# Performance work log

Hardware: AMD Instinct MI355X
Metric: run time of the kernel (lower is better)

The kernel has to match this reference:

```python
import jax, jax.numpy as jnp
import numpy as np


def _gtconv(A, w):
    # A: [E,N,N], w: [C,E,1,1]; torch: sum(A * softmax(w, dim=1), dim=1) -> [C,N,N]
    s = jax.nn.softmax(w[:, :, 0, 0], axis=1)  # [C,E]
    return jnp.einsum('enm,ce->cnm', A, s)


def _norm_row(H):
    # row-normalize (H + I): D^-1 (H + I)
    n = H.shape[0]
    H = H + jnp.eye(n, dtype=H.dtype)
    deg = jnp.sum(H, axis=1)
    deg = jnp.where(deg <= 1e-10, 1.0, deg)
    return H / deg[:, None]


def _sgc(feature, adj):
    # D^-1/2 (adj + 2I) D^-1/2 @ feature  (diag scaling, same math as torch's dense mm with diag)
    n = adj.shape[0]
    adj = adj + 2.0 * jnp.eye(n, dtype=adj.dtype)
    deg = jnp.sum(adj, axis=1)
    deg = jnp.where(deg <= 1e-10, 1.0, deg)
    dinv = deg ** -0.5
    adj = adj * dinv[:, None] * dinv[None, :]
    return adj @ feature


def setup_inputs() -> dict:
    key = jax.random.key(0)
    ks = jax.random.split(key, 20)
    E, C, N, D, P, F = 5, 2, 3000, 1000, 2000, 128
    inp = {
        'A': jax.random.uniform(ks[0], (E, N, N), dtype=jnp.float32),
        'DTI': jax.random.uniform(ks[1], (N, N), dtype=jnp.float32),
        'drug_structure': jax.random.normal(ks[2], (D, F), dtype=jnp.float32),
        'protein_structure': jax.random.normal(ks[3], (P, F), dtype=jnp.float32),
        'gt_w0a': jax.random.normal(ks[4], (C, E, 1, 1), dtype=jnp.float32),
        'gt_w0b': jax.random.normal(ks[5], (C, E, 1, 1), dtype=jnp.float32),
        'gt_w1': jax.random.normal(ks[6], (C, E, 1, 1), dtype=jnp.float32),
        'a_param': jnp.ones((C + 1, 1, 1), dtype=jnp.float32),
        'drug_num': D,
        'protein_num': P,
    }
    lin_keys = jax.random.split(ks[7], 12)
    names = ['wd1', 'bd1', 'wd2', 'bd2', 'wd3', 'bd3', 'wp1', 'bp1', 'wp2', 'bp2', 'wp3', 'bp3']
    for i, nm in enumerate(names):
        shp = (F, F) if nm.startswith('w') else (F,)
        inp[nm] = jax.random.normal(lin_keys[i], shp, dtype=jnp.float32) * 0.05
    return inp


def reference(A, DTI, drug_structure, protein_structure, gt_w0a, gt_w0b, gt_w1,
              wd1, bd1, wd2, bd2, wd3, bd3, wp1, bp1, wp2, bp2, wp3, bp3,
              a_param, drug_num, protein_num):
    relu = jax.nn.relu
    drug = relu(drug_structure @ wd1.T + bd1)
    drug = relu(drug @ wd2.T + bd2)
    drug = relu(drug @ wd3.T + bd3)
    prot = relu(protein_structure @ wp1.T + bp1)
    prot = relu(prot @ wp2.T + bp2)
    prot = relu(prot @ wp3.T + bp3)
    feature = jnp.concatenate([drug, prot], axis=0)  # [N,128]

    # GT layers: layer 0 (first=True), layer 1 (first=False)
    a0 = _gtconv(A, gt_w0a)  # [C,N,N]
    b0 = _gtconv(A, gt_w0b)
    H = jnp.matmul(a0, b0)  # bmm
    H = jax.vmap(_norm_row)(H)
    H = jnp.matmul(H, _gtconv(A, gt_w1))

    adj = H  # H[:, :N, :N] is a no-op here
    X_conv1 = _sgc(_sgc(feature, DTI), DTI)
    chs = jax.vmap(lambda a_: _sgc(_sgc(feature, a_), a_))(adj)  # [C,N,128]

    C = adj.shape[0]
    if C == 1:
        X_conv3 = chs
    else:
        order = [0, 1]
        for i in range(2, C):
            order = [i] + order  # torch prepends X_tem for i>=2
        X_conv3 = chs[jnp.array(order)]

    X_conv = jnp.concatenate([X_conv1[None], X_conv3], axis=0)  # [C+1,N,128]
    att = jax.nn.softmax(a_param, axis=0)  # [C+1,1,1]
    conv_sum = jnp.sum(att * X_conv, axis=0)  # [N,128]

    drug_feature = conv_sum[:drug_num]
    protein_feature = conv_sum[drug_num:]
    y = jax.nn.sigmoid(drug_feature @ protein_feature.T)  # [D,P]
    return y
```

## Files before the change

### kernel.cpp

```cpp
#include <hip/hip_runtime.h>
#include <hip/hip_bf16.h>

typedef __attribute__((ext_vector_type(8))) __bf16 bf16x8;
typedef __attribute__((ext_vector_type(4))) float floatx4;

#define NVALID 3000
#define NPAD   3072
#define FEA    128
#define ZSPLIT 8
#define KCHUNK 384
#define PSTRIDE 393216
#define SLOT   ((size_t)ZSPLIT * PSTRIDE)

__device__ __forceinline__ void gload16(const void* g, void* l) {
    __builtin_amdgcn_global_load_lds(
        (const __attribute__((address_space(1))) void*)g,
        (__attribute__((address_space(3))) void*)l,
        16, 0, 0);
}

__device__ __forceinline__ float b2f(__hip_bfloat16 h) { return __bfloat162float(h); }

__global__ __launch_bounds__(256) void mlp_fused(
    const float* __restrict__ Xd, const float* __restrict__ Xp,
    const float* __restrict__ Wd1, const float* __restrict__ bd1,
    const float* __restrict__ Wd2, const float* __restrict__ bd2,
    const float* __restrict__ Wd3, const float* __restrict__ bd3,
    const float* __restrict__ Wp1, const float* __restrict__ bp1,
    const float* __restrict__ Wp2, const float* __restrict__ bp2,
    const float* __restrict__ Wp3, const float* __restrict__ bp3,
    float* __restrict__ Y)
{
    const bool isP = blockIdx.x >= 125;
    const float* X  = isP ? Xp : Xd;
    const float* W1 = isP ? Wp1 : Wd1; const float* b1 = isP ? bp1 : bd1;
    const float* W2 = isP ? Wp2 : Wd2; const float* b2 = isP ? bp2 : bd2;
    const float* W3 = isP ? Wp3 : Wd3; const float* b3 = isP ? bp3 : bd3;
    const int m0loc = (isP ? (blockIdx.x - 125) : blockIdx.x) * 8;
    const int m0out = blockIdx.x * 8;

    __shared__ float S0[8][128], S1[8][128];
    const int t = threadIdx.x;
    for (int s2 = t; s2 < 1024; s2 += 256) {
        int r = s2 >> 7, ii = s2 & 127;
        S0[r][ii] = X[(size_t)(m0loc + r) * 128 + ii];
    }
    __syncthreads();
    const int o = t & 127, rh = t >> 7;

    {
        float a0 = 0.f, a1 = 0.f, a2 = 0.f, a3 = 0.f;
        const float* wr = W1 + (size_t)o * 128;
        for (int i = 0; i < 128; ++i) {
            float w = wr[i];
            a0 += S0[rh + 0][i] * w; a1 += S0[rh + 2][i] * w;
            a2 += S0[rh + 4][i] * w; a3 += S0[rh + 6][i] * w;
        }
        float bo = b1[o];
        S1[rh + 0][o] = fmaxf(a0 + bo, 0.f);
        S1[rh + 2][o] = fmaxf(a1 + bo, 0.f);
        S1[rh + 4][o] = fmaxf(a2 + bo, 0.f);
        S1[rh + 6][o] = fmaxf(a3 + bo, 0.f);
    }
    __syncthreads();
    {
        float a0 = 0.f, a1 = 0.f, a2 = 0.f, a3 = 0.f;
        const float* wr = W2 + (size_t)o * 128;
        for (int i = 0; i < 128; ++i) {
            float w = wr[i];
            a0 += S1[rh + 0][i] * w; a1 += S1[rh + 2][i] * w;
            a2 += S1[rh + 4][i] * w; a3 += S1[rh + 6][i] * w;
        }
        float bo = b2[o];
        S0[rh + 0][o] = fmaxf(a0 + bo, 0.f);
        S0[rh + 2][o] = fmaxf(a1 + bo, 0.f);
        S0[rh + 4][o] = fmaxf(a2 + bo, 0.f);
        S0[rh + 6][o] = fmaxf(a3 + bo, 0.f);
    }
    __syncthreads();
    {
        float a0 = 0.f, a1 = 0.f, a2 = 0.f, a3 = 0.f;
        const float* wr = W3 + (size_t)o * 128;
        for (int i = 0; i < 128; ++i) {
            float w = wr[i];
            a0 += S0[rh + 0][i] * w; a1 += S0[rh + 2][i] * w;
            a2 += S0[rh + 4][i] * w; a3 += S0[rh + 6][i] * w;
        }
        float bo = b3[o];
        Y[(size_t)(m0out + rh + 0) * 128 + o] = fmaxf(a0 + bo, 0.f);
        Y[(size_t)(m0out + rh + 2) * 128 + o] = fmaxf(a1 + bo, 0.f);
        Y[(size_t)(m0out + rh + 4) * 128 + o] = fmaxf(a2 + bo, 0.f);
        Y[(size_t)(m0out + rh + 6) * 128 + o] = fmaxf(a3 + bo, 0.f);
    }
}

__device__ __forceinline__ void softmax5(const float* __restrict__ w, float* s)
{
    float m = w[0];
    #pragma unroll
    for (int e = 1; e < 5; ++e) m = fmaxf(m, w[e]);
    float sum = 0.f;
    #pragma unroll
    for (int e = 0; e < 5; ++e) { s[e] = __expf(w[e] - m); sum += s[e]; }
    float r = 1.f / sum;
    #pragma unroll
    for (int e = 0; e < 5; ++e) s[e] *= r;
}

__global__ __launch_bounds__(384) void gtconv_fused(
    const float* __restrict__ A, const float* __restrict__ w0a,
    const float* __restrict__ w0b, const float* __restrict__ w1,
    __hip_bfloat16* __restrict__ a00, __hip_bfloat16* __restrict__ b00,
    __hip_bfloat16* __restrict__ g10,
    __hip_bfloat16* __restrict__ a01, __hip_bfloat16* __restrict__ b01,
    __hip_bfloat16* __restrict__ g11,
    float* __restrict__ r1v)
{
    float sw[6][5];
    softmax5(w0a + 0, sw[0]); softmax5(w0b + 0, sw[1]); softmax5(w1 + 0, sw[2]);
    softmax5(w0a + 5, sw[3]); softmax5(w0b + 5, sw[4]); softmax5(w1 + 5, sw[5]);

    const int i  = blockIdx.x;
    const int t  = threadIdx.x;
    const int j0 = t * 8;
    float acc[6][8] = {};
    if (i < NVALID && j0 < NVALID) {
        #pragma unroll
        for (int e = 0; e < 5; ++e) {
            const float* Ae = A + (size_t)e * 9000000 + (size_t)i * 3000 + j0;
            float4 v0 = *reinterpret_cast<const float4*>(Ae);
            float4 v1 = *reinterpret_cast<const float4*>(Ae + 4);
            float x[8] = { v0.x, v0.y, v0.z, v0.w, v1.x, v1.y, v1.z, v1.w };
            #pragma unroll
            for (int m = 0; m < 6; ++m) {
                float se = sw[m][e];
                #pragma unroll
                for (int u = 0; u < 8; ++u) acc[m][u] += se * x[u];
            }
        }
    }
    __hip_bfloat16* dsts[6] = { a00, b00, g10, a01, b01, g11 };
    const size_t base = (size_t)i * NPAD + j0;
    float rs[4];
    #pragma unroll
    for (int m = 0; m < 6; ++m) {
        __align__(16) __hip_bfloat16 h[8];
        float s = 0.f;
        #pragma unroll
        for (int u = 0; u < 8; ++u) {
            h[u] = __float2bfloat16(acc[m][u]);
            s += b2f(h[u]);
        }
        *reinterpret_cast<uint4*>(&dsts[m][base]) = *reinterpret_cast<const uint4*>(h);
        if (m == 1) rs[0] = s; else if (m == 2) rs[1] = s;
        else if (m == 4) rs[2] = s; else if (m == 5) rs[3] = s;
    }
    __shared__ float red[6][4];
    #pragma unroll
    for (int q = 0; q < 4; ++q) {
        float s = rs[q];
        #pragma unroll
        for (int off = 32; off > 0; off >>= 1) s += __shfl_down(s, off);
        if ((t & 63) == 0) red[t >> 6][q] = s;
    }
    __syncthreads();
    if (t == 0) {
        #pragma unroll
        for (int q = 0; q < 4; ++q) {
            float s = red[0][q] + red[1][q] + red[2][q]
                    + red[3][q] + red[4][q] + red[5][q];
            r1v[(size_t)q * NPAD + i] = s;
        }
    }
}

__global__ __launch_bounds__(256) void matvec_degA(
    const __hip_bfloat16* __restrict__ a0_0, const __hip_bfloat16* __restrict__ a0_1,
    const __hip_bfloat16* __restrict__ b0_0, const __hip_bfloat16* __restrict__ b0_1,
    const float* __restrict__ r1v,
    float* __restrict__ dinv2, float* __restrict__ mv12)
{
    const int y = blockIdx.y;
    const __hip_bfloat16* M = (y == 0) ? a0_0 : (y == 1) ? a0_1 : (y == 2) ? b0_0 : b0_1;
    const float* v = (y == 0) ? r1v : (y == 1) ? r1v + 2 * NPAD
                   : (y == 2) ? r1v + NPAD : r1v + 3 * NPAD;
    const size_t i = blockIdx.x;
    const int t = threadIdx.x;
    const __hip_bfloat16* row = M + i * NPAD;
    float s = 0.f;
    for (int k = t * 8; k < NPAD; k += 2048) {
        uint4 u = *reinterpret_cast<const uint4*>(&row[k]);
        const unsigned short* us = reinterpret_cast<const unsigned short*>(&u);
        #pragma unroll
        for (int e = 0; e < 8; ++e)
            s += __uint_as_float(((unsigned int)us[e]) << 16) * v[k + e];
    }
    #pragma unroll
    for (int off = 32; off > 0; off >>= 1) s += __shfl_down(s, off);
    __shared__ float red[4];
    if ((t & 63) == 0) red[t >> 6] = s;
    __syncthreads();
    if (t == 0) {
        float tot = red[0] + red[1] + red[2] + red[3];
        if (y < 2) dinv2[(size_t)y * NPAD + i] = 1.f / (tot + 1.f);
        else       mv12[(size_t)(y - 2) * NPAD + i] = tot;
    }
}

__global__ __launch_bounds__(256) void matvec_degB(
    const __hip_bfloat16* __restrict__ a0_0, const __hip_bfloat16* __restrict__ a0_1,
    const float* __restrict__ mv12, const float* __restrict__ dinv2,
    const float* __restrict__ r1v, float* __restrict__ rsv2)
{
    const int c = blockIdx.y;
    const __hip_bfloat16* M = c ? a0_1 : a0_0;
    const float* v = mv12 + (size_t)c * NPAD;
    const float* add = r1v + (size_t)(2 * c + 1) * NPAD;
    const size_t i = blockIdx.x;
    const int t = threadIdx.x;
    const __hip_bfloat16* row = M + i * NPAD;
    float s = 0.f;
    for (int k = t * 8; k < NPAD; k += 2048) {
        uint4 u = *reinterpret_cast<const uint4*>(&row[k]);
        const unsigned short* us = reinterpret_cast<const unsigned short*>(&u);
        #pragma unroll
        for (int e = 0; e < 8; ++e)
            s += __uint_as_float(((unsigned int)us[e]) << 16) * v[k + e];
    }
    #pragma unroll
    for (int off = 32; off > 0; off >>= 1) s += __shfl_down(s, off);
    __shared__ float red[4];
    if ((t & 63) == 0) red[t >> 6] = s;
    __syncthreads();
    if (t == 0) {
        float tot = red[0] + red[1] + red[2] + red[3];
        rsv2[(size_t)c * NPAD + i] =
            rsqrtf(dinv2[(size_t)c * NPAD + i] * (tot + add[i]) + 2.f);
    }
}

__global__ __launch_bounds__(256) void rowdeg_f32(
    const float* __restrict__ src, float* __restrict__ outv)
{
    const int i = blockIdx.x, t = threadIdx.x;
    float s = 0.f;
    if (i < NVALID) {
        const float* row = src + (size_t)i * 3000;
        for (int j4 = t; j4 < 750; j4 += 256) {
            float4 v = *reinterpret_cast<const float4*>(row + j4 * 4);
            s += v.x + v.y + v.z + v.w;
        }
    }
    #pragma unroll
    for (int off = 32; off > 0; off >>= 1) s += __shfl_down(s, off);
    __shared__ float red[4];
    if ((t & 63) == 0) red[t >> 6] = s;
    __syncthreads();
    if (t == 0) {
        float tot = red[0] + red[1] + red[2] + red[3];
        outv[i] = rsqrtf(tot + 2.f);
    }
}

__global__ __launch_bounds__(256) void scale_cast_f32(
    const float* __restrict__ src, int lds_, int nvalid,
    const float* __restrict__ vec, __hip_bfloat16* __restrict__ dst)
{
    const int i = blockIdx.y;
    const int j0 = (blockIdx.x * 256 + threadIdx.x) * 4;
    const float vi = vec[i];
    float v[4];
    if (i < nvalid && j0 + 3 < nvalid) {
        float4 f = *reinterpret_cast<const float4*>(src + (size_t)i * lds_ + j0);
        v[0] = f.x; v[1] = f.y; v[2] = f.z; v[3] = f.w;
    } else {
        #pragma unroll
        for (int u = 0; u < 4; ++u) {
            int j = j0 + u;
            v[u] = (i < nvalid && j < nvalid) ? src[(size_t)i * lds_ + j] : 0.f;
        }
    }
    #pragma unroll
    for (int u = 0; u < 4; ++u) {
        int j = j0 + u;
        if (j == i && i < nvalid) v[u] += 2.f;
        v[u] *= vi * vec[j];
    }
    __align__(8) __hip_bfloat16 h[4];
    #pragma unroll
    for (int u = 0; u < 4; ++u) h[u] = __float2bfloat16(v[u]);
    *reinterpret_cast<uint2*>(&dst[(size_t)i * NPAD + j0]) =
        *reinterpret_cast<const uint2*>(h);
}

__global__ __launch_bounds__(256) void transpose_feat(
    const float* __restrict__ X, int nvalid, __hip_bfloat16* __restrict__ XT)
{
    __shared__ float Ts[32][33];
    const int k0 = blockIdx.x * 32, n0 = blockIdx.y * 32;
    const int t = threadIdx.x, tr = t >> 5, tc = t & 31;
    #pragma unroll
    for (int p = 0; p < 4; ++p) {
        int k = k0 + tr + p * 8;
        Ts[tr + p * 8][tc] = (k < nvalid) ? X[(size_t)k * 128 + n0 + tc] : 0.f;
    }
    __syncthreads();
    #pragma unroll
    for (int p = 0; p < 4; ++p) {
        int n = tr + p * 8;
        XT[(size_t)(n0 + n) * NPAD + k0 + tc] = __float2bfloat16(Ts[tc][n]);
    }
}

__global__ __launch_bounds__(256) void scale_colsT2(
    const __hip_bfloat16* __restrict__ XT, const float* __restrict__ rsv2,
    __hip_bfloat16* __restrict__ W0T_0, __hip_bfloat16* __restrict__ W0T_1)
{
    const int c = blockIdx.z;
    const float* s = rsv2 + (size_t)c * NPAD;
    __hip_bfloat16* W0T = c ? W0T_1 : W0T_0;
    const int f = blockIdx.y;
    const int k0 = (blockIdx.x * 256 + threadIdx.x) * 8;
    if (k0 >= NPAD) return;
    uint4 u = *reinterpret_cast<const uint4*>(&XT[(size_t)f * NPAD + k0]);
    const unsigned short* us = reinterpret_cast<const unsigned short*>(&u);
    __align__(16) __hip_bfloat16 h[8];
    #pragma unroll
    for (int e = 0; e < 8; ++e) {
        float x = __uint_as_float(((unsigned int)us[e]) << 16);
        h[e] = __float2bfloat16(x * s[k0 + e]);
    }
    *reinterpret_cast<uint4*>(&W0T[(size_t)f * NPAD + k0]) =
        *reinterpret_cast<const uint4*>(h);
}

__global__ __launch_bounds__(256, 3) void gemm_bt_batch(
    const __hip_bfloat16* __restrict__ A0, const __hip_bfloat16* __restrict__ B0,
    const __hip_bfloat16* __restrict__ A1, const __hip_bfloat16* __restrict__ B1,
    const __hip_bfloat16* __restrict__ A2, const __hip_bfloat16* __restrict__ B2,
    __hip_bfloat16* __restrict__ part)
{
    const int b  = blockIdx.z / ZSPLIT;
    const int zz = blockIdx.z % ZSPLIT;
    const __hip_bfloat16* A  = (b == 0) ? A0 : (b == 1) ? A1 : A2;
    const __hip_bfloat16* BT = (b == 0) ? B0 : (b == 1) ? B1 : B2;
    __hip_bfloat16* C = part + (size_t)b * SLOT + (size_t)zz * PSTRIDE;

    __shared__ __align__(16) __hip_bfloat16 As[128 * 32];
    __shared__ __align__(16) __hip_bfloat16 Bs[128 * 32];
    const int t = threadIdx.x;
    const int lane = t & 63;
    const int w = t >> 6;
    const int wm = w >> 1, wn = w & 1;
    const int tm = blockIdx.y;
    const int kbeg = zz * KCHUNK;

    const int srow = lane >> 2;
    const int skg  = (lane & 3) * 8;
    const __hip_bfloat16* Ag = A  + (size_t)(tm * 128 + w * 32 + srow) * NPAD + skg;
    const __hip_bfloat16* Bg = BT + (size_t)(w * 32 + srow) * NPAD + skg;
    __hip_bfloat16* Al0 = &As[w * 1024];
    __hip_bfloat16* Al1 = &As[w * 1024 + 512];
    __hip_bfloat16* Bl0 = &Bs[w * 1024];
    __hip_bfloat16* Bl1 = &Bs[w * 1024 + 512];

    floatx4 acc[4][4] = {};

    for (int k0 = kbeg; k0 < kbeg + KCHUNK; k0 += 32) {
        __syncthreads();
        gload16(Ag + k0,             Al0);
        gload16(Ag + 16 * NPAD + k0, Al1);
        gload16(Bg + k0,             Bl0);
        gload16(Bg + 16 * NPAD + k0, Bl1);
        __syncthreads();

        bf16x8 af[4], bfv[4];
        const int koff = (lane >> 4) * 8;
        #pragma unroll
        for (int mi = 0; mi < 4; ++mi)
            af[mi] = *reinterpret_cast<const bf16x8*>(
                &As[(wm * 64 + mi * 16 + (lane & 15)) * 32 + koff]);
        #pragma unroll
        for (int ni = 0; ni < 4; ++ni)
            bfv[ni] = *reinterpret_cast<const bf16x8*>(
                &Bs[(wn * 64 + ni * 16 + (lane & 15)) * 32 + koff]);
        #pragma unroll
        for (int mi = 0; mi < 4; ++mi)
            #pragma unroll
            for (int ni = 0; ni < 4; ++ni)
                acc[mi][ni] = __builtin_amdgcn_mfma_f32_16x16x32_bf16(
                    af[mi], bfv[ni], acc[mi][ni], 0, 0, 0);
    }

    const int r0 = tm * 128 + wm * 64 + ((lane >> 4) << 2);
    const int c0 = wn * 64 + (lane & 15);
    #pragma unroll
    for (int mi = 0; mi < 4; ++mi)
        #pragma unroll
        for (int ni = 0; ni < 4; ++ni)
            #pragma unroll
            for (int r = 0; r < 4; ++r)
                C[(size_t)(r0 + mi * 16 + r) * 128 + c0 + ni * 16] =
                    __float2bfloat16(acc[mi][ni][r]);
}

__global__ __launch_bounds__(256, 3) void gemm_sig(
    const __hip_bfloat16* __restrict__ A, const __hip_bfloat16* __restrict__ BT,
    float* __restrict__ C, int Kchunk, int lda, int ldb, int ldc,
    int Mvalid, int Nvalid)
{
    __shared__ __align__(16) __hip_bfloat16 As[128 * 32];
    __shared__ __align__(16) __hip_bfloat16 Bs[128 * 32];
    const int t = threadIdx.x;
    const int lane = t & 63;
    const int w = t >> 6;
    const int wm = w >> 1, wn = w & 1;
    const int tm = blockIdx.y, tn = blockIdx.x;

    const int srow = lane >> 2;
    const int skg  = (lane & 3) * 8;
    const __hip_bfloat16* Ag = A  + (size_t)(tm * 128 + w * 32 + srow) * lda + skg;
    const __hip_bfloat16* Bg = BT + (size_t)(tn * 128 + w * 32 + srow) * ldb + skg;
    __hip_bfloat16* Al0 = &As[w * 1024];
    __hip_bfloat16* Al1 = &As[w * 1024 + 512];
    __hip_bfloat16* Bl0 = &Bs[w * 1024];
    __hip_bfloat16* Bl1 = &Bs[w * 1024 + 512];

    floatx4 acc[4][4] = {};

    for (int k0 = 0; k0 < Kchunk; k0 += 32) {
        __syncthreads();
        gload16(Ag + k0,            Al0);
        gload16(Ag + 16 * lda + k0, Al1);
        gload16(Bg + k0,            Bl0);
        gload16(Bg + 16 * ldb + k0, Bl1);
        __syncthreads();

        bf16x8 af[4], bfv[4];
        const int koff = (lane >> 4) * 8;
        #pragma unroll
        for (int mi = 0; mi < 4; ++mi)
            af[mi] = *reinterpret_cast<const bf16x8*>(
                &As[(wm * 64 + mi * 16 + (lane & 15)) * 32 + koff]);
        #pragma unroll
        for (int ni = 0; ni < 4; ++ni)
            bfv[ni] = *reinterpret_cast<const bf16x8*>(
                &Bs[(wn * 64 + ni * 16 + (lane & 15)) * 32 + koff]);
        #pragma unroll
        for (int mi = 0; mi < 4; ++mi)
            #pragma unroll
            for (int ni = 0; ni < 4; ++ni)
                acc[mi][ni] = __builtin_amdgcn_mfma_f32_16x16x32_bf16(
                    af[mi], bfv[ni], acc[mi][ni], 0, 0, 0);
    }

    const int r0 = tm * 128 + wm * 64 + ((lane >> 4) << 2);
    const int c0 = tn * 128 + wn * 64 + (lane & 15);
    #pragma unroll
    for (int mi = 0; mi < 4; ++mi)
        #pragma unroll
        for (int ni = 0; ni < 4; ++ni) {
            const int col = c0 + ni * 16;
            #pragma unroll
            for (int r = 0; r < 4; ++r) {
                const int row = r0 + mi * 16 + r;
                if (row < Mvalid && col < Nvalid)
                    C[(size_t)row * ldc + col] =
                        1.f / (1.f + __expf(-acc[mi][ni][r]));
            }
        }
}

__global__ __launch_bounds__(256) void reduce_trans_b(
    const __hip_bfloat16* __restrict__ part,
    __hip_bfloat16* __restrict__ X0, __hip_bfloat16* __restrict__ X1,
    __hip_bfloat16* __restrict__ X2,
    __hip_bfloat16* __restrict__ R0, __hip_bfloat16* __restrict__ R1,
    __hip_bfloat16* __restrict__ R2,
    const float* __restrict__ ap, float* __restrict__ conv)
{
    const int b = blockIdx.z;
    const __hip_bfloat16* Pp = part + (size_t)b * SLOT;
    const int k0 = blockIdx.x * 32, n0 = blockIdx.y * 32;
    const int t = threadIdx.x, tr = t >> 5, tc = t & 31;

    if (b == 0 && conv != nullptr) {
        float a0 = ap[0], a1 = ap[1], a2 = ap[2];
        float m = fmaxf(a0, fmaxf(a1, a2));
        float e0 = __expf(a0 - m), e1 = __expf(a1 - m), e2 = __expf(a2 - m);
        float att0 = e0 / (e0 + e1 + e2);
        #pragma unroll
        for (int p = 0; p < 4; ++p) {
            int i = k0 + tr + p * 8;
            float s = 0.f;
            #pragma unroll
            for (int z = 0; z < ZSPLIT; ++z)
                s += b2f(Pp[(size_t)z * PSTRIDE + (size_t)i * 128 + n0 + tc]);
            conv[(size_t)i * 128 + n0 + tc] = att0 * s;
        }
        return;
    }

    __hip_bfloat16* XT = (b == 0) ? X0 : (b == 1) ? X1 : X2;
    __hip_bfloat16* Rm = (b == 0) ? R0 : (b == 1) ? R1 : R2;
    __shared__ float Ts[32][33];
    #pragma unroll
    for (int p = 0; p < 4; ++p) {
        int i = k0 + tr + p * 8;
        float s = 0.f;
        #pragma unroll
        for (int z = 0; z < ZSPLIT; ++z)
            s += b2f(Pp[(size_t)z * PSTRIDE + (size_t)i * 128 + n0 + tc]);
        Ts[tr + p * 8][tc] = s;
        if (Rm) Rm[(size_t)i * 128 + n0 + tc] = __float2bfloat16(s);
    }
    __syncthreads();
    #pragma unroll
    for (int p = 0; p < 4; ++p) {
        int n = tr + p * 8;
        XT[(size_t)(n0 + n) * NPAD + k0 + tc] = __float2bfloat16(Ts[tc][n]);
    }
}

__global__ __launch_bounds__(256) void combine_mid2(
    const __hip_bfloat16* __restrict__ part,
    const __hip_bfloat16* __restrict__ Zrm0, const __hip_bfloat16* __restrict__ Zrm1,
    const float* __restrict__ X,
    const float* __restrict__ rsv2, const float* __restrict__ dinv2,
    __hip_bfloat16* __restrict__ WpT0, __hip_bfloat16* __restrict__ WpT1,
    __hip_bfloat16* __restrict__ Wprm0, __hip_bfloat16* __restrict__ Wprm1)
{
    const int c = blockIdx.z;
    const __hip_bfloat16* Vp = part + (size_t)c * SLOT;
    const __hip_bfloat16* Zrm = c ? Zrm1 : Zrm0;
    const float* sv = rsv2 + (size_t)c * NPAD;
    const float* dv = dinv2 + (size_t)c * NPAD;
    __hip_bfloat16* WpT  = c ? WpT1 : WpT0;
    __hip_bfloat16* Wprm = c ? Wprm1 : Wprm0;

    __shared__ float Ts[32][33];
    const int k0 = blockIdx.x * 32, n0 = blockIdx.y * 32;
    const int t = threadIdx.x, tr = t >> 5, tc = t & 31;
    #pragma unroll
    for (int p = 0; p < 4; ++p) {
        int i = k0 + tr + p * 8;
        int f = n0 + tc;
        float vsum = b2f(Zrm[(size_t)i * 128 + f]);
        #pragma unroll
        for (int z = 0; z < ZSPLIT; ++z)
            vsum += b2f(Vp[(size_t)z * PSTRIDE + (size_t)i * 128 + f]);
        float x  = (i < NVALID) ? X[(size_t)i * 128 + f] : 0.f;
        float si = sv[i];
        float out1 = si * dv[i] * vsum + 2.f * si * si * x;
        float wv = si * out1;
        Ts[tr + p * 8][tc] = wv;
        Wprm[(size_t)i * 128 + f] = __float2bfloat16(wv);
    }
    __syncthreads();
    #pragma unroll
    for (int p = 0; p < 4; ++p) {
        int n = tr + p * 8;
        WpT[(size_t)(n0 + n) * NPAD + k0 + tc] = __float2bfloat16(Ts[tc][n]);
    }
}

__global__ __launch_bounds__(256) void combine_att2(
    const __hip_bfloat16* __restrict__ part,
    const __hip_bfloat16* __restrict__ Zrm0, const __hip_bfloat16* __restrict__ Zrm1,
    const __hip_bfloat16* __restrict__ Wprm0, const __hip_bfloat16* __restrict__ Wprm1,
    const float* __restrict__ rsv2, const float* __restrict__ dinv2,
    const float* __restrict__ ap, float* __restrict__ conv)
{
    const int idx = blockIdx.x * 256 + threadIdx.x;
    const int i = idx >> 7;
    float v0 = b2f(Zrm0[idx]);
    float v1 = b2f(Zrm1[idx]);
    #pragma unroll
    for (int z = 0; z < ZSPLIT; ++z) {
        v0 += b2f(part[(size_t)z * PSTRIDE + idx]);
        v1 += b2f(part[SLOT + (size_t)z * PSTRIDE + idx]);
    }
    float s0 = rsv2[i],        d0 = dinv2[i];
    float s1 = rsv2[NPAD + i], d1 = dinv2[NPAD + i];
    float o0 = s0 * d0 * v0 + 2.f * s0 * b2f(Wprm0[idx]);
    float o1 = s1 * d1 * v1 + 2.f * s1 * b2f(Wprm1[idx]);
    float a0 = ap[0], a1 = ap[1], a2 = ap[2];
    float m = fmaxf(a0, fmaxf(a1, a2));
    float e0 = __expf(a0 - m), e1 = __expf(a1 - m), e2 = __expf(a2 - m);
    float inv = 1.f / (e0 + e1 + e2);
    conv[idx] += (e1 * inv) * o0 + (e2 * inv) * o1;
}

__global__ __launch_bounds__(256) void cast_split(
    const float* __restrict__ acc, __hip_bfloat16* __restrict__ dF,
    __hip_bfloat16* __restrict__ pF)
{
    const int idx = blockIdx.x * 256 + threadIdx.x;
    if (idx < 1024 * 128) {
        int r = idx >> 7;
        dF[idx] = __float2bfloat16(r < 1000 ? acc[idx] : 0.f);
    } else {
        int j = idx - 1024 * 128;
        int r = j >> 7;
        pF[j] = __float2bfloat16(r < 2000 ? acc[(size_t)(1000 + r) * 128 + (j & 127)] : 0.f);
    }
}

extern "C" void kernel_launch(void* const* d_in, const int* in_sizes, int n_in,
                              void* d_out, int out_size, void* d_ws, size_t ws_size,
                              hipStream_t stream)
{
    const float* A     = (const float*)d_in[0];
    const float* DTI   = (const float*)d_in[1];
    const float* drugS = (const float*)d_in[2];
    const float* protS = (const float*)d_in[3];
    const float* w0a   = (const float*)d_in[4];
    const float* w0b   = (const float*)d_in[5];
    const float* w1g   = (const float*)d_in[6];
    const float* ap    = (const float*)d_in[7];
    const float* wd1 = (const float*)d_in[10]; const float* bd1 = (const float*)d_in[11];
    const float* wd2 = (const float*)d_in[12]; const float* bd2 = (const float*)d_in[13];
    const float* wd3 = (const float*)d_in[14]; const float* bd3 = (const float*)d_in[15];
    const float* wp1 = (const float*)d_in[16]; const float* bp1 = (const float*)d_in[17];
    const float* wp2 = (const float*)d_in[18]; const float* bp2 = (const float*)d_in[19];
    const float* wp3 = (const float*)d_in[20]; const float* bp3 = (const float*)d_in[21];
    float* out = (float*)d_out;

    const size_t SQ_BF  = (size_t)NPAD * NPAD * 2;
    const size_t PAN_BF = (size_t)128 * NPAD * 2;
    char* p = (char*)d_ws;
    auto alloc = [&](size_t sz) { char* r = p; p += (sz + 255) & ~(size_t)255; return r; };
    __hip_bfloat16* sdti = (__hip_bfloat16*)alloc(SQ_BF);
    __hip_bfloat16* a0c[2], *b0c[2], *g1c[2];
    for (int c = 0; c < 2; ++c) {
        a0c[c] = (__hip_bfloat16*)alloc(SQ_BF);
        b0c[c] = (__hip_bfloat16*)alloc(SQ_BF);
        g1c[c] = (__hip_bfloat16*)alloc(SQ_BF);
    }
    __hip_bfloat16* part = (__hip_bfloat16*)alloc((size_t)3 * SLOT * 2);
    float* r1v   = (float*)alloc((size_t)4 * NPAD * 4);
    float* dinv2 = (float*)alloc((size_t)2 * NPAD * 4);
    float* mv12  = (float*)alloc((size_t)2 * NPAD * 4);
    float* rsv2  = (float*)alloc((size_t)2 * NPAD * 4);
    float* degv  = (float*)alloc((size_t)NPAD * 4);
    float* fb    = (float*)alloc((size_t)NPAD * 128 * 4);
    float* conv  = (float*)alloc((size_t)NPAD * 128 * 4);
    __hip_bfloat16* XTF  = (__hip_bfloat16*)alloc(PAN_BF);
    __hip_bfloat16* XT2  = (__hip_bfloat16*)alloc(PAN_BF);
    __hip_bfloat16* W0T_0 = (__hip_bfloat16*)alloc(PAN_BF);
    __hip_bfloat16* W0T_1 = (__hip_bfloat16*)alloc(PAN_BF);
    __hip_bfloat16* ZT_0  = (__hip_bfloat16*)alloc(PAN_BF);
    __hip_bfloat16* ZT_1  = (__hip_bfloat16*)alloc(PAN_BF);
    __hip_bfloat16* Zrm_0 = (__hip_bfloat16*)alloc(PAN_BF);
    __hip_bfloat16* Zrm_1 = (__hip_bfloat16*)alloc(PAN_BF);
    __hip_bfloat16* UT_0  = (__hip_bfloat16*)alloc(PAN_BF);
    __hip_bfloat16* UT_1  = (__hip_bfloat16*)alloc(PAN_BF);
    __hip_bfloat16* WpT_0 = (__hip_bfloat16*)alloc(PAN_BF);
    __hip_bfloat16* WpT_1 = (__hip_bfloat16*)alloc(PAN_BF);
    __hip_bfloat16* Wprm_0 = (__hip_bfloat16*)alloc(PAN_BF);
    __hip_bfloat16* Wprm_1 = (__hip_bfloat16*)alloc(PAN_BF);
    __hip_bfloat16* dF = (__hip_bfloat16*)alloc((size_t)1024 * 128 * 2);
    __hip_bfloat16* pF = (__hip_bfloat16*)alloc((size_t)2048 * 128 * 2);
    if ((size_t)(p - (char*)d_ws) > ws_size) return;

    mlp_fused<<<375, 256, 0, stream>>>(drugS, protS,
        wd1, bd1, wd2, bd2, wd3, bd3, wp1, bp1, wp2, bp2, wp3, bp3, fb);
    transpose_feat<<<dim3(96, 4), 256, 0, stream>>>(fb, 3000, XTF);

    gtconv_fused<<<NPAD, 384, 0, stream>>>(A, w0a, w0b, w1g,
        a0c[0], b0c[0], g1c[0], a0c[1], b0c[1], g1c[1], r1v);

    rowdeg_f32<<<NPAD, 256, 0, stream>>>(DTI, degv);
    scale_cast_f32<<<dim3(3, NPAD), 256, 0, stream>>>(DTI, 3000, 3000, degv, sdti);

    matvec_degA<<<dim3(NPAD, 4), 256, 0, stream>>>(a0c[0], a0c[1], b0c[0], b0c[1],
        r1v, dinv2, mv12);
    matvec_degB<<<dim3(NPAD, 2), 256, 0, stream>>>(a0c[0], a0c[1], mv12, dinv2, r1v, rsv2);
    scale_colsT2<<<dim3(2, 128, 2), 256, 0, stream>>>(XTF, rsv2, W0T_0, W0T_1);

    gemm_bt_batch<<<dim3(1, 24, 3 * ZSPLIT), 256, 0, stream>>>(
        sdti, XTF, g1c[0], W0T_0, g1c[1], W0T_1, part);
    reduce_trans_b<<<dim3(96, 4, 3), 256, 0, stream>>>(part,
        XT2, ZT_0, ZT_1, nullptr, Zrm_0, Zrm_1, nullptr, nullptr);

    gemm_bt_batch<<<dim3(1, 24, 3 * ZSPLIT), 256, 0, stream>>>(
        sdti, XT2, b0c[0], ZT_0, b0c[1], ZT_1, part);
    reduce_trans_b<<<dim3(96, 4, 3), 256, 0, stream>>>(part,
        nullptr, UT_0, UT_1, nullptr, nullptr, nullptr, ap, conv);

    gemm_bt_batch<<<dim3(1, 24, 2 * ZSPLIT), 256, 0, stream>>>(
        a0c[0], UT_0, a0c[1], UT_1, nullptr, nullptr, part);
    combine_mid2<<<dim3(96, 4, 2), 256, 0, stream>>>(part, Zrm_0, Zrm_1, fb,
        rsv2, dinv2, WpT_0, WpT_1, Wprm_0, Wprm_1);

    gemm_bt_batch<<<dim3(1, 24, 2 * ZSPLIT), 256, 0, stream>>>(
        g1c[0], WpT_0, g1c[1], WpT_1, nullptr, nullptr, part);
    reduce_trans_b<<<dim3(96, 4, 2), 256, 0, stream>>>(part,
        ZT_0, ZT_1, nullptr, Zrm_0, Zrm_1, nullptr, nullptr, nullptr);
    gemm_bt_batch<<<dim3(1, 24, 2 * ZSPLIT), 256, 0, stream>>>(
        b0c[0], ZT_0, b0c[1], ZT_1, nullptr, nullptr, part);
    reduce_trans_b<<<dim3(96, 4, 2), 256, 0, stream>>>(part,
        UT_0, UT_1, nullptr, nullptr, nullptr, nullptr, nullptr, nullptr);
    gemm_bt_batch<<<dim3(1, 24, 2 * ZSPLIT), 256, 0, stream>>>(
        a0c[0], UT_0, a0c[1], UT_1, nullptr, nullptr, part);
    combine_att2<<<1500, 256, 0, stream>>>(part, Zrm_0, Zrm_1, Wprm_0, Wprm_1,
        rsv2, dinv2, ap, conv);

    cast_split<<<1536, 256, 0, stream>>>(conv, dF, pF);
    gemm_sig<<<dim3(16, 8), 256, 0, stream>>>(dF, pF, out, 128, 128, 128, 2000, 1000, 2000);
}
```

Before: 269.8 us.

## Keep chain intermediates in transposed panel layout, drop per-step transposes

```diff
diff --git a/kernel.cpp b/kernel.cpp
--- a/kernel.cpp
+++ b/kernel.cpp
@@ -334,16 +334,16 @@
         *reinterpret_cast<const uint4*>(h);
 }
 
-__global__ __launch_bounds__(256, 3) void gemm_bt_batch(
-    const __hip_bfloat16* __restrict__ A0, const __hip_bfloat16* __restrict__ B0,
-    const __hip_bfloat16* __restrict__ A1, const __hip_bfloat16* __restrict__ B1,
-    const __hip_bfloat16* __restrict__ A2, const __hip_bfloat16* __restrict__ B2,
+__global__ __launch_bounds__(256, 3) void gemm_pan_batch(
+    const __hip_bfloat16* __restrict__ P0, const __hip_bfloat16* __restrict__ M0,
+    const __hip_bfloat16* __restrict__ P1, const __hip_bfloat16* __restrict__ M1,
+    const __hip_bfloat16* __restrict__ P2, const __hip_bfloat16* __restrict__ M2,
     __hip_bfloat16* __restrict__ part)
 {
     const int b  = blockIdx.z / ZSPLIT;
     const int zz = blockIdx.z % ZSPLIT;
-    const __hip_bfloat16* A  = (b == 0) ? A0 : (b == 1) ? A1 : A2;
-    const __hip_bfloat16* BT = (b == 0) ? B0 : (b == 1) ? B1 : B2;
+    const __hip_bfloat16* P = (b == 0) ? P0 : (b == 1) ? P1 : P2;
+    const __hip_bfloat16* M = (b == 0) ? M0 : (b == 1) ? M1 : M2;
     __hip_bfloat16* C = part + (size_t)b * SLOT + (size_t)zz * PSTRIDE;
 
     __shared__ __align__(16) __hip_bfloat16 As[128 * 32];
@@ -352,13 +352,13 @@
     const int lane = t & 63;
     const int w = t >> 6;
     const int wm = w >> 1, wn = w & 1;
-    const int tm = blockIdx.y;
+    const int tn = blockIdx.x;
     const int kbeg = zz * KCHUNK;
 
     const int srow = lane >> 2;
     const int skg  = (lane & 3) * 8;
-    const __hip_bfloat16* Ag = A  + (size_t)(tm * 128 + w * 32 + srow) * NPAD + skg;
-    const __hip_bfloat16* Bg = BT + (size_t)(w * 32 + srow) * NPAD + skg;
+    const __hip_bfloat16* Ag = P + (size_t)(w * 32 + srow) * NPAD + skg;
+    const __hip_bfloat16* Bg = M + (size_t)(tn * 128 + w * 32 + srow) * NPAD + skg;
     __hip_bfloat16* Al0 = &As[w * 1024];
     __hip_bfloat16* Al1 = &As[w * 1024 + 512];
     __hip_bfloat16* Bl0 = &Bs[w * 1024];
@@ -392,15 +392,15 @@
                     af[mi], bfv[ni], acc[mi][ni], 0, 0, 0);
     }
 
-    const int r0 = tm * 128 + wm * 64 + ((lane >> 4) << 2);
-    const int c0 = wn * 64 + (lane & 15);
+    const int r0 = wm * 64 + ((lane >> 4) << 2);
+    const int c0 = tn * 128 + wn * 64 + (lane & 15);
     #pragma unroll
     for (int mi = 0; mi < 4; ++mi)
         #pragma unroll
         for (int ni = 0; ni < 4; ++ni)
             #pragma unroll
             for (int r = 0; r < 4; ++r)
-                C[(size_t)(r0 + mi * 16 + r) * 128 + c0 + ni * 16] =
+                C[(size_t)(r0 + mi * 16 + r) * NPAD + c0 + ni * 16] =
                     __float2bfloat16(acc[mi][ni][r]);
 }
 
@@ -471,124 +471,139 @@
         }
 }
 
-__global__ __launch_bounds__(256) void reduce_trans_b(
+__global__ __launch_bounds__(256) void reduce_sum_b(
     const __hip_bfloat16* __restrict__ part,
-    __hip_bfloat16* __restrict__ X0, __hip_bfloat16* __restrict__ X1,
-    __hip_bfloat16* __restrict__ X2,
-    __hip_bfloat16* __restrict__ R0, __hip_bfloat16* __restrict__ R1,
-    __hip_bfloat16* __restrict__ R2,
-    const float* __restrict__ ap, float* __restrict__ conv)
-{
-    const int b = blockIdx.z;
+    __hip_bfloat16* __restrict__ O0, __hip_bfloat16* __restrict__ O1,
+    __hip_bfloat16* __restrict__ O2)
+{
+    const int b = blockIdx.y;
+    __hip_bfloat16* O = (b == 0) ? O0 : (b == 1) ? O1 : O2;
+    if (!O) return;
     const __hip_bfloat16* Pp = part + (size_t)b * SLOT;
-    const int k0 = blockIdx.x * 32, n0 = blockIdx.y * 32;
+    const size_t idx = ((size_t)blockIdx.x * 256 + threadIdx.x) * 8;
+    float s[8] = {};
+    #pragma unroll
+    for (int z = 0; z < ZSPLIT; ++z) {
+        uint4 u = *reinterpret_cast<const uint4*>(&Pp[(size_t)z * PSTRIDE + idx]);
+        const unsigned short* us = reinterpret_cast<const unsigned short*>(&u);
+        #pragma unroll
+        for (int e = 0; e < 8; ++e)
+            s[e] += __uint_as_float(((unsigned int)us[e]) << 16);
+    }
+    __align__(16) __hip_bfloat16 h[8];
+    #pragma unroll
+    for (int e = 0; e < 8; ++e) h[e] = __float2bfloat16(s[e]);
+    *reinterpret_cast<uint4*>(&O[idx]) = *reinterpret_cast<const uint4*>(h);
+}
+
+__global__ __launch_bounds__(256) void reduce_att_T(
+    const __hip_bfloat16* __restrict__ part, const float* __restrict__ ap,
+    float* __restrict__ conv)
+{
+    __shared__ float Ts[32][33];
+    const int i0 = blockIdx.x * 32, f0 = blockIdx.y * 32;
     const int t = threadIdx.x, tr = t >> 5, tc = t & 31;
-
-    if (b == 0 && conv != nullptr) {
-        float a0 = ap[0], a1 = ap[1], a2 = ap[2];
-        float m = fmaxf(a0, fmaxf(a1, a2));
-        float e0 = __expf(a0 - m), e1 = __expf(a1 - m), e2 = __expf(a2 - m);
-        float att0 = e0 / (e0 + e1 + e2);
-        #pragma unroll
-        for (int p = 0; p < 4; ++p) {
-            int i = k0 + tr + p * 8;
-            float s = 0.f;
-            #pragma unroll
-            for (int z = 0; z < ZSPLIT; ++z)
-                s += b2f(Pp[(size_t)z * PSTRIDE + (size_t)i * 128 + n0 + tc]);
-            conv[(size_t)i * 128 + n0 + tc] = att0 * s;
-        }
-        return;
-    }
-
-    __hip_bfloat16* XT = (b == 0) ? X0 : (b == 1) ? X1 : X2;
-    __hip_bfloat16* Rm = (b == 0) ? R0 : (b == 1) ? R1 : R2;
-    __shared__ float Ts[32][33];
+    float a0 = ap[0], a1 = ap[1], a2 = ap[2];
+    float m = fmaxf(a0, fmaxf(a1, a2));
+    float e0 = __expf(a0 - m), e1 = __expf(a1 - m), e2 = __expf(a2 - m);
+    float att0 = e0 / (e0 + e1 + e2);
     #pragma unroll
     for (int p = 0; p < 4; ++p) {
-        int i = k0 + tr + p * 8;
+        int f = f0 + tr + p * 8;
         float s = 0.f;
         #pragma unroll
         for (int z = 0; z < ZSPLIT; ++z)
-            s += b2f(Pp[(size_t)z * PSTRIDE + (size_t)i * 128 + n0 + tc]);
+            s += b2f(part[(size_t)z * PSTRIDE + (size_t)f * NPAD + i0 + tc]);
         Ts[tr + p * 8][tc] = s;
-        if (Rm) Rm[(size_t)i * 128 + n0 + tc] = __float2bfloat16(s);
     }
     __syncthreads();
     #pragma unroll
     for (int p = 0; p < 4; ++p) {
-        int n = tr + p * 8;
-        XT[(size_t)(n0 + n) * NPAD + k0 + tc] = __float2bfloat16(Ts[tc][n]);
+        int i = i0 + tr + p * 8;
+        conv[(size_t)i * 128 + f0 + tc] = att0 * Ts[tc][tr + p * 8];
     }
 }
 
 __global__ __launch_bounds__(256) void combine_mid2(
     const __hip_bfloat16* __restrict__ part,
-    const __hip_bfloat16* __restrict__ Zrm0, const __hip_bfloat16* __restrict__ Zrm1,
-    const float* __restrict__ X,
+    const __hip_bfloat16* __restrict__ Z0, const __hip_bfloat16* __restrict__ Z1,
+    const __hip_bfloat16* __restrict__ XTF,
     const float* __restrict__ rsv2, const float* __restrict__ dinv2,
-    __hip_bfloat16* __restrict__ WpT0, __hip_bfloat16* __restrict__ WpT1,
-    __hip_bfloat16* __restrict__ Wprm0, __hip_bfloat16* __restrict__ Wprm1)
-{
-    const int c = blockIdx.z;
+    __hip_bfloat16* __restrict__ Wp0, __hip_bfloat16* __restrict__ Wp1)
+{
+    const int c = blockIdx.y;
     const __hip_bfloat16* Vp = part + (size_t)c * SLOT;
-    const __hip_bfloat16* Zrm = c ? Zrm1 : Zrm0;
+    const __hip_bfloat16* Z  = c ? Z1 : Z0;
     const float* sv = rsv2 + (size_t)c * NPAD;
     const float* dv = dinv2 + (size_t)c * NPAD;
-    __hip_bfloat16* WpT  = c ? WpT1 : WpT0;
-    __hip_bfloat16* Wprm = c ? Wprm1 : Wprm0;
-
-    __shared__ float Ts[32][33];
-    const int k0 = blockIdx.x * 32, n0 = blockIdx.y * 32;
-    const int t = threadIdx.x, tr = t >> 5, tc = t & 31;
-    #pragma unroll
-    for (int p = 0; p < 4; ++p) {
-        int i = k0 + tr + p * 8;
-        int f = n0 + tc;
-        float vsum = b2f(Zrm[(size_t)i * 128 + f]);
-        #pragma unroll
-        for (int z = 0; z < ZSPLIT; ++z)
-            vsum += b2f(Vp[(size_t)z * PSTRIDE + (size_t)i * 128 + f]);
-        float x  = (i < NVALID) ? X[(size_t)i * 128 + f] : 0.f;
-        float si = sv[i];
-        float out1 = si * dv[i] * vsum + 2.f * si * si * x;
-        float wv = si * out1;
-        Ts[tr + p * 8][tc] = wv;
-        Wprm[(size_t)i * 128 + f] = __float2bfloat16(wv);
-    }
-    __syncthreads();
-    #pragma unroll
-    for (int p = 0; p < 4; ++p) {
-        int n = tr + p * 8;
-        WpT[(size_t)(n0 + n) * NPAD + k0 + tc] = __float2bfloat16(Ts[tc][n]);
-    }
-}
-
-__global__ __launch_bounds__(256) void combine_att2(
+    __hip_bfloat16* Wp = c ? Wp1 : Wp0;
+
+    const size_t idx = ((size_t)blockIdx.x * 256 + threadIdx.x) * 8;
+    const int i = (int)(idx % NPAD);
+    float s[8] = {};
+    #pragma unroll
+    for (int z = 0; z < ZSPLIT; ++z) {
+        uint4 u = *reinterpret_cast<const uint4*>(&Vp[(size_t)z * PSTRIDE + idx]);
+        const unsigned short* us = reinterpret_cast<const unsigned short*>(&u);
+        #pragma unroll
+        for (int e = 0; e < 8; ++e)
+            s[e] += __uint_as_float(((unsigned int)us[e]) << 16);
+    }
+    uint4 uz = *reinterpret_cast<const uint4*>(&Z[idx]);
+    uint4 ux = *reinterpret_cast<const uint4*>(&XTF[idx]);
+    const unsigned short* usz = reinterpret_cast<const unsigned short*>(&uz);
+    const unsigned short* usx = reinterpret_cast<const unsigned short*>(&ux);
+    __align__(16) __hip_bfloat16 h[8];
+    #pragma unroll
+    for (int e = 0; e < 8; ++e) {
+        float vsum = s[e] + __uint_as_float(((unsigned int)usz[e]) << 16);
+        float x    = __uint_as_float(((unsigned int)usx[e]) << 16);
+        float si = sv[i + e], di = dv[i + e];
+        float out1 = si * di * vsum + 2.f * si * si * x;
+        h[e] = __float2bfloat16(si * out1);
+    }
+    *reinterpret_cast<uint4*>(&Wp[idx]) = *reinterpret_cast<const uint4*>(h);
+}
+
+__global__ __launch_bounds__(256) void combine_att2_T(
     const __hip_bfloat16* __restrict__ part,
-    const __hip_bfloat16* __restrict__ Zrm0, const __hip_bfloat16* __restrict__ Zrm1,
-    const __hip_bfloat16* __restrict__ Wprm0, const __hip_bfloat16* __restrict__ Wprm1,
+    const __hip_bfloat16* __restrict__ Z2_0, const __hip_bfloat16* __restrict__ Z2_1,
+    const __hip_bfloat16* __restrict__ Wp0, const __hip_bfloat16* __restrict__ Wp1,
     const float* __restrict__ rsv2, const float* __restrict__ dinv2,
     const float* __restrict__ ap, float* __restrict__ conv)
 {
-    const int idx = blockIdx.x * 256 + threadIdx.x;
-    const int i = idx >> 7;
-    float v0 = b2f(Zrm0[idx]);
-    float v1 = b2f(Zrm1[idx]);
-    #pragma unroll
-    for (int z = 0; z < ZSPLIT; ++z) {
-        v0 += b2f(part[(size_t)z * PSTRIDE + idx]);
-        v1 += b2f(part[SLOT + (size_t)z * PSTRIDE + idx]);
-    }
-    float s0 = rsv2[i],        d0 = dinv2[i];
-    float s1 = rsv2[NPAD + i], d1 = dinv2[NPAD + i];
-    float o0 = s0 * d0 * v0 + 2.f * s0 * b2f(Wprm0[idx]);
-    float o1 = s1 * d1 * v1 + 2.f * s1 * b2f(Wprm1[idx]);
+    __shared__ float Ts[32][33];
+    const int i0 = blockIdx.x * 32, f0 = blockIdx.y * 32;
+    const int t = threadIdx.x, tr = t >> 5, tc = t & 31;
     float a0 = ap[0], a1 = ap[1], a2 = ap[2];
     float m = fmaxf(a0, fmaxf(a1, a2));
     float e0 = __expf(a0 - m), e1 = __expf(a1 - m), e2 = __expf(a2 - m);
     float inv = 1.f / (e0 + e1 + e2);
-    conv[idx] += (e1 * inv) * o0 + (e2 * inv) * o1;
+    float att1 = e1 * inv, att2 = e2 * inv;
+    const int i = i0 + tc;
+    float s0i = rsv2[i],        d0i = dinv2[i];
+    float s1i = rsv2[NPAD + i], d1i = dinv2[NPAD + i];
+    #pragma unroll
+    for (int p = 0; p < 4; ++p) {
+        int f = f0 + tr + p * 8;
+        size_t fi = (size_t)f * NPAD + i;
+        float v0 = b2f(Z2_0[fi]);
+        float v1 = b2f(Z2_1[fi]);
+        #pragma unroll
+        for (int z = 0; z < ZSPLIT; ++z) {
+            v0 += b2f(part[(size_t)z * PSTRIDE + fi]);
+            v1 += b2f(part[SLOT + (size_t)z * PSTRIDE + fi]);
+        }
+        float o0 = s0i * d0i * v0 + 2.f * s0i * b2f(Wp0[fi]);
+        float o1 = s1i * d1i * v1 + 2.f * s1i * b2f(Wp1[fi]);
+        Ts[tr + p * 8][tc] = att1 * o0 + att2 * o1;
+    }
+    __syncthreads();
+    #pragma unroll
+    for (int p = 0; p < 4; ++p) {
+        int i2 = i0 + tr + p * 8;
+        conv[(size_t)i2 * 128 + f0 + tc] += Ts[tc][tr + p * 8];
+    }
 }
 
 __global__ __launch_bounds__(256) void cast_split(
@@ -649,16 +664,12 @@
     __hip_bfloat16* XT2  = (__hip_bfloat16*)alloc(PAN_BF);
     __hip_bfloat16* W0T_0 = (__hip_bfloat16*)alloc(PAN_BF);
     __hip_bfloat16* W0T_1 = (__hip_bfloat16*)alloc(PAN_BF);
-    __hip_bfloat16* ZT_0  = (__hip_bfloat16*)alloc(PAN_BF);
-    __hip_bfloat16* ZT_1  = (__hip_bfloat16*)alloc(PAN_BF);
-    __hip_bfloat16* Zrm_0 = (__hip_bfloat16*)alloc(PAN_BF);
-    __hip_bfloat16* Zrm_1 = (__hip_bfloat16*)alloc(PAN_BF);
-    __hip_bfloat16* UT_0  = (__hip_bfloat16*)alloc(PAN_BF);
-    __hip_bfloat16* UT_1  = (__hip_bfloat16*)alloc(PAN_BF);
-    __hip_bfloat16* WpT_0 = (__hip_bfloat16*)alloc(PAN_BF);
-    __hip_bfloat16* WpT_1 = (__hip_bfloat16*)alloc(PAN_BF);
-    __hip_bfloat16* Wprm_0 = (__hip_bfloat16*)alloc(PAN_BF);
-    __hip_bfloat16* Wprm_1 = (__hip_bfloat16*)alloc(PAN_BF);
+    __hip_bfloat16* Z_0  = (__hip_bfloat16*)alloc(PAN_BF);
+    __hip_bfloat16* Z_1  = (__hip_bfloat16*)alloc(PAN_BF);
+    __hip_bfloat16* U_0  = (__hip_bfloat16*)alloc(PAN_BF);
+    __hip_bfloat16* U_1  = (__hip_bfloat16*)alloc(PAN_BF);
+    __hip_bfloat16* Wp_0 = (__hip_bfloat16*)alloc(PAN_BF);
+    __hip_bfloat16* Wp_1 = (__hip_bfloat16*)alloc(PAN_BF);
     __hip_bfloat16* dF = (__hip_bfloat16*)alloc((size_t)1024 * 128 * 2);
     __hip_bfloat16* pF = (__hip_bfloat16*)alloc((size_t)2048 * 128 * 2);
     if ((size_t)(p - (char*)d_ws) > ws_size) return;
@@ -678,32 +689,29 @@
     matvec_degB<<<dim3(NPAD, 2), 256, 0, stream>>>(a0c[0], a0c[1], mv12, dinv2, r1v, rsv2);
     scale_colsT2<<<dim3(2, 128, 2), 256, 0, stream>>>(XTF, rsv2, W0T_0, W0T_1);
 
-    gemm_bt_batch<<<dim3(1, 24, 3 * ZSPLIT), 256, 0, stream>>>(
-        sdti, XTF, g1c[0], W0T_0, g1c[1], W0T_1, part);
-    reduce_trans_b<<<dim3(96, 4, 3), 256, 0, stream>>>(part,
-        XT2, ZT_0, ZT_1, nullptr, Zrm_0, Zrm_1, nullptr, nullptr);
-
-    gemm_bt_batch<<<dim3(1, 24, 3 * ZSPLIT), 256, 0, stream>>>(
-        sdti, XT2, b0c[0], ZT_0, b0c[1], ZT_1, part);
-    reduce_trans_b<<<dim3(96, 4, 3), 256, 0, stream>>>(part,
-        nullptr, UT_0, UT_1, nullptr, nullptr, nullptr, ap, conv);
-
-    gemm_bt_batch<<<dim3(1, 24, 2 * ZSPLIT), 256, 0, stream>>>(
-        a0c[0], UT_0, a0c[1], UT_1, nullptr, nullptr, part);
-    combine_mid2<<<dim3(96, 4, 2), 256, 0, stream>>>(part, Zrm_0, Zrm_1, fb,
-        rsv2, dinv2, WpT_0, WpT_1, Wprm_0, Wprm_1);
-
-    gemm_bt_batch<<<dim3(1, 24, 2 * ZSPLIT), 256, 0, stream>>>(
-        g1c[0], WpT_0, g1c[1], WpT_1, nullptr, nullptr, part);
-    reduce_trans_b<<<dim3(96, 4, 2), 256, 0, stream>>>(part,
-        ZT_0, ZT_1, nullptr, Zrm_0, Zrm_1, nullptr, nullptr, nullptr);
-    gemm_bt_batch<<<dim3(1, 24, 2 * ZSPLIT), 256, 0, stream>>>(
-        b0c[0], ZT_0, b0c[1], ZT_1, nullptr, nullptr, part);
-    reduce_trans_b<<<dim3(96, 4, 2), 256, 0, stream>>>(part,
-        UT_0, UT_1, nullptr, nullptr, nullptr, nullptr, nullptr, nullptr);
-    gemm_bt_batch<<<dim3(1, 24, 2 * ZSPLIT), 256, 0, stream>>>(
-        a0c[0], UT_0, a0c[1], UT_1, nullptr, nullptr, part);
-    combine_att2<<<1500, 256, 0, stream>>>(part, Zrm_0, Zrm_1, Wprm_0, Wprm_1,
+    gemm_pan_batch<<<dim3(24, 1, 3 * ZSPLIT), 256, 0, stream>>>(
+        XTF, sdti, W0T_0, g1c[0], W0T_1, g1c[1], part);
+    reduce_sum_b<<<dim3(192, 3), 256, 0, stream>>>(part, XT2, Z_0, Z_1);
+
+    gemm_pan_batch<<<dim3(24, 1, 3 * ZSPLIT), 256, 0, stream>>>(
+        XT2, sdti, Z_0, b0c[0], Z_1, b0c[1], part);
+    reduce_att_T<<<dim3(96, 4), 256, 0, stream>>>(part, ap, conv);
+    reduce_sum_b<<<dim3(192, 2), 256, 0, stream>>>(part + SLOT, U_0, U_1, nullptr);
+
+    gemm_pan_batch<<<dim3(24, 1, 2 * ZSPLIT), 256, 0, stream>>>(
+        U_0, a0c[0], U_1, a0c[1], nullptr, nullptr, part);
+    combine_mid2<<<dim3(192, 2), 256, 0, stream>>>(part, Z_0, Z_1, XTF,
+        rsv2, dinv2, Wp_0, Wp_1);
+
+    gemm_pan_batch<<<dim3(24, 1, 2 * ZSPLIT), 256, 0, stream>>>(
+        Wp_0, g1c[0], Wp_1, g1c[1], nullptr, nullptr, part);
+    reduce_sum_b<<<dim3(192, 2), 256, 0, stream>>>(part, Z_0, Z_1, nullptr);
+    gemm_pan_batch<<<dim3(24, 1, 2 * ZSPLIT), 256, 0, stream>>>(
+        Z_0, b0c[0], Z_1, b0c[1], nullptr, nullptr, part);
+    reduce_sum_b<<<dim3(192, 2), 256, 0, stream>>>(part, U_0, U_1, nullptr);
+    gemm_pan_batch<<<dim3(24, 1, 2 * ZSPLIT), 256, 0, stream>>>(
+        U_0, a0c[0], U_1, a0c[1], nullptr, nullptr, part);
+    combine_att2_T<<<dim3(96, 4), 256, 0, stream>>>(part, Z_0, Z_1, Wp_0, Wp_1,
         rsv2, dinv2, ap, conv);
 
     cast_split<<<1536, 256, 0, stream>>>(conv, dF, pF);
```

After: 267.4 us. About the same (-0.9%).
